# Optimization experiments

Hardware: AMD Instinct MI355X
Metric: run time of the kernel (lower is better)

Reference implementation:

```python
import jax, jax.numpy as jnp
import numpy as np

S = 2        # subsample_rate
EPS = 1e-5   # BatchNorm eps


def maxpool(x, k):
    B, C, H, W = x.shape
    return x.reshape(B, C, H // k, k, W // k, k).max(axis=(3, 5))


def conv1x1(x, w, b):
    # x: [B,C,H,W], w: [O,C], b: [O]
    return jnp.einsum('bchw,oc->bohw', x, w) + b[None, :, None, None]


def upsample_bilinear_ac(y, s):
    # torch nn.Upsample(mode='bilinear', scale_factor=s, align_corners=True)
    B, C, h, w = y.shape
    H, W = h * s, w * s
    ri = jnp.arange(H, dtype=jnp.float32) * ((h - 1) / (H - 1))
    ci = jnp.arange(W, dtype=jnp.float32) * ((w - 1) / (W - 1))
    r0 = jnp.floor(ri).astype(jnp.int32); r1 = jnp.minimum(r0 + 1, h - 1)
    c0 = jnp.floor(ci).astype(jnp.int32); c1 = jnp.minimum(c0 + 1, w - 1)
    wr = (ri - r0)[None, None, :, None]
    wc = (ci - c0)[None, None, None, :]
    top = y[:, :, r0, :] * (1.0 - wr) + y[:, :, r1, :] * wr
    return top[:, :, :, c0] * (1.0 - wc) + top[:, :, :, c1] * wc


def setup_inputs() -> dict:
    key = jax.random.key(0)
    ks = jax.random.split(key, 12)
    B, C, IC, H, W = 4, 256, 128, 192, 192
    sc = 0.05  # keep attention logits in a sane range
    x = jax.random.normal(ks[0], (B, C, H, W), jnp.float32)
    g_w = jax.random.normal(ks[1], (IC, C), jnp.float32) * sc
    g_b = jax.random.normal(ks[2], (IC,), jnp.float32) * sc
    theta_w = jax.random.normal(ks[3], (IC, C), jnp.float32) * sc
    theta_b = jax.random.normal(ks[4], (IC,), jnp.float32) * sc
    phi_w = jax.random.normal(ks[5], (IC, C), jnp.float32) * sc
    phi_b = jax.random.normal(ks[6], (IC,), jnp.float32) * sc
    W_w = jax.random.normal(ks[7], (C, IC, 3, 3), jnp.float32) * sc
    W_b = jax.random.normal(ks[8], (C,), jnp.float32) * sc
    bn_gamma = jnp.ones((C,), jnp.float32)
    bn_beta = jnp.zeros((C,), jnp.float32)
    bn_mean = jax.random.normal(ks[9], (C,), jnp.float32) * sc
    bn_var = jax.random.uniform(ks[10], (C,), jnp.float32) + 0.5
    return dict(x=x, g_w=g_w, g_b=g_b, theta_w=theta_w, theta_b=theta_b,
                phi_w=phi_w, phi_b=phi_b, W_w=W_w, W_b=W_b,
                bn_gamma=bn_gamma, bn_beta=bn_beta, bn_mean=bn_mean, bn_var=bn_var)


def reference(x, g_w, g_b, theta_w, theta_b, phi_w, phi_b, W_w, W_b,
              bn_gamma, bn_beta, bn_mean, bn_var):
    B, C, H, Wd = x.shape
    IC = g_w.shape[0]
    xp = maxpool(x, S)                               # [B,C,H/S,W/S]
    theta = conv1x1(xp, theta_w, theta_b)            # [B,IC,h,w]
    g = maxpool(conv1x1(xp, g_w, g_b), 2)            # [B,IC,h/2,w/2]
    phi = maxpool(conv1x1(xp, phi_w, phi_b), 2)      # [B,IC,h/2,w/2]
    h, w = theta.shape[2], theta.shape[3]
    th = theta.reshape(B, IC, h * w).transpose(0, 2, 1)   # [B,Nt,IC]
    ph = phi.reshape(B, IC, -1)                           # [B,IC,Np]
    gx = g.reshape(B, IC, -1).transpose(0, 2, 1)          # [B,Np,IC]
    f = jnp.einsum('bnc,bcm->bnm', th, ph)                # [B,Nt,Np]
    a = jax.nn.softmax(f, axis=-1)
    y = jnp.einsum('bnm,bmc->bnc', a, gx)                 # [B,Nt,IC]
    y = y.transpose(0, 2, 1).reshape(B, IC, h, w)
    y = upsample_bilinear_ac(y, S)                        # [B,IC,H,W]
    wy = jax.lax.conv_general_dilated(
        y, W_w, (1, 1), ((1, 1), (1, 1)),
        dimension_numbers=('NCHW', 'OIHW', 'NCHW')) + W_b[None, :, None, None]
    inv = bn_gamma / jnp.sqrt(bn_var + EPS)
    wy = (wy - bn_mean[None, :, None, None]) * inv[None, :, None, None] + bn_beta[None, :, None, None]
    return (wy + x, wy)
```

## Files before the change

kernel.cpp:

```cpp
#include <hip/hip_runtime.h>
#include <hip/hip_bf16.h>
#include <math.h>

#define B_   4
#define C_   256
#define ICH  128
#define H_   192
#define W_   192
#define hs   96
#define ws2  96
#define HW   (hs*ws2)
#define HP   48
#define WP   48
#define NP   (HP*WP)
#define EPSB 1e-5f
#define PADW 194
#define TOT  ((size_t)B_*C_*H_*W_)

#define QB 64
#define KB 64
#define NT (NP/KB)
#define SM_OFF 20.0f

using bf16x8 = __attribute__((ext_vector_type(8))) short;
using f32x4  = __attribute__((ext_vector_type(4))) float;
using f32x16 = __attribute__((ext_vector_type(16))) float;

#define OFF_XPB   ((size_t)0)
#define OFF_THB   ((size_t)4718592)
#define OFF_PHB   ((size_t)7077888)
#define OFF_GBT   ((size_t)7667712)
#define OFF_WB3   ((size_t)8257536)
#define OFF_Y96N  ((size_t)8306688)
#define OFF_ST    ((size_t)13025280)
#define OFF_WT    ((size_t)13025792)
#define OFF_YPAD  ((size_t)13173248)

static __device__ __forceinline__ float b2f(unsigned short u) {
  union { unsigned int i; float f; } c; c.i = (unsigned int)u << 16; return c.f;
}

__global__ __launch_bounds__(256) void k_pool_nhwc(const float* __restrict__ x,
                                                   __hip_bfloat16* __restrict__ xpb) {
  int idx = blockIdx.x * 256 + threadIdx.x;
  int cg = idx & 31;
  int n  = (idx >> 5) % HW;
  int b  = idx / (32 * HW);
  int pi = n / ws2, pj = n % ws2;
  const float* xb = x + (((size_t)b * C_ + cg * 8) * H_ + 2 * pi) * W_ + 2 * pj;
  union { ushort u[8]; uint4 v; } pk;
#pragma unroll
  for (int cc = 0; cc < 8; ++cc) {
    const float* s = xb + (size_t)cc * H_ * W_;
    float v = fmaxf(fmaxf(s[0], s[1]), fmaxf(s[W_], s[W_ + 1]));
    __hip_bfloat16 hv = __float2bfloat16(v);
    pk.u[cc] = *(ushort*)&hv;
  }
  *(uint4*)(xpb + ((size_t)b * HW + n) * C_ + cg * 8) = pk.v;
}

__global__ __launch_bounds__(256) void k_wprep(const float* __restrict__ tw,
                                               const float* __restrict__ gw,
                                               const float* __restrict__ pw,
                                               __hip_bfloat16* __restrict__ wb3) {
  int idx = blockIdx.x * 256 + threadIdx.x;
  int set = idx >> 15; int rem = idx & 32767;
  const float* src = set == 0 ? tw : (set == 1 ? gw : pw);
  wb3[idx] = __float2bfloat16(src[rem]);
}

__global__ __launch_bounds__(256) void k_qkv2(
    const __hip_bfloat16* __restrict__ xpb,
    const __hip_bfloat16* __restrict__ wb3,
    const float* __restrict__ tb, const float* __restrict__ gb_,
    const float* __restrict__ pb_,
    __hip_bfloat16* __restrict__ thb,
    __hip_bfloat16* __restrict__ gbt,
    __hip_bfloat16* __restrict__ phb) {
  __shared__ __align__(16) char ldsX[96 * 512];
  int t = threadIdx.x;
  int lane = t & 63, li = lane & 15, g4 = lane >> 4;
  int wid = t >> 6;
  int wave_o = wid >> 1, wave_n = wid & 1;
  int ih = blockIdx.x;
  int i  = ih >> 1, half = ih & 1;
  int b  = blockIdx.y;
  const size_t xbase = (size_t)b * HW * C_;

#pragma unroll
  for (int rr = 0; rr < 12; ++rr) {
    int e = rr * 256 + t;
    int j = e >> 5, c8 = e & 31;
    int sc8 = c8 ^ (j & 7);
    int pix = (2 * i + (j & 1)) * ws2 + half * 48 + (j >> 1);
    __builtin_amdgcn_global_load_lds(
        (const __attribute__((address_space(1))) void*)(xpb + xbase + (size_t)pix * C_ + sc8 * 8),
        (__attribute__((address_space(3))) void*)(ldsX + (rr * 256 + (t & 192)) * 16),
        16, 0, 0);
  }
  asm volatile("s_waitcnt vmcnt(0)" ::: "memory");
  __builtin_amdgcn_s_barrier();

  for (int set = 0; set < 3; ++set) {
    const __hip_bfloat16* wset = wb3 + (size_t)set * 128 * 256;
    const float* bias = set == 0 ? tb : (set == 1 ? gb_ : pb_);
    f32x4 acc[4][3];
#pragma unroll
    for (int fo = 0; fo < 4; ++fo)
#pragma unroll
      for (int fq = 0; fq < 3; ++fq) acc[fo][fq] = (f32x4){0.f, 0.f, 0.f, 0.f};

    for (int step = 0; step < 4; ++step) {
      bf16x8 af[4][2];
#pragma unroll
      for (int fo = 0; fo < 4; ++fo)
#pragma unroll
        for (int ks = 0; ks < 2; ++ks) {
          int o = wave_o * 64 + fo * 16 + li;
          af[fo][ks] = *(const bf16x8*)(wset + (size_t)o * C_ + step * 64 + ks * 32 + g4 * 8);
        }
#pragma unroll
      for (int ks = 0; ks < 2; ++ks)
#pragma unroll
        for (int fq = 0; fq < 3; ++fq) {
          int j = wave_n * 48 + fq * 16 + li;
          int sl = (step * 8 + ks * 4 + g4) ^ (j & 7);
          bf16x8 bx = *(const bf16x8*)(ldsX + j * 512 + sl * 16);
#pragma unroll
          for (int fo = 0; fo < 4; ++fo)
            acc[fo][fq] = __builtin_amdgcn_mfma_f32_16x16x32_bf16(af[fo][ks], bx, acc[fo][fq], 0, 0, 0);
        }
    }

    if (set == 0) {
#pragma unroll
      for (int fo = 0; fo < 4; ++fo) {
        int ob = wave_o * 64 + fo * 16 + g4 * 4;
#pragma unroll
        for (int fq = 0; fq < 3; ++fq) {
          int j = wave_n * 48 + fq * 16 + li;
          int pix = (2 * i + (j & 1)) * ws2 + half * 48 + (j >> 1);
          union { ushort u[4]; uint2 v; } pk;
#pragma unroll
          for (int r = 0; r < 4; ++r) {
            __hip_bfloat16 hv = __float2bfloat16(acc[fo][fq][r] + bias[ob + r]);
            pk.u[r] = *(ushort*)&hv;
          }
          *(uint2*)(thb + ((size_t)b * HW + pix) * ICH + ob) = pk.v;
        }
      }
    } else {
#pragma unroll
      for (int fo = 0; fo < 4; ++fo) {
        int ob = wave_o * 64 + fo * 16 + g4 * 4;
#pragma unroll
        for (int fq = 0; fq < 3; ++fq) {
          float pv[4];
#pragma unroll
          for (int r = 0; r < 4; ++r) {
            float p = acc[fo][fq][r];
            p = fmaxf(p, __shfl_xor(p, 1, 64));
            p = fmaxf(p, __shfl_xor(p, 2, 64));
            pv[r] = p;
          }
          if ((li & 3) == 0) {
            int pc = half * 24 + wave_n * 12 + fq * 4 + (li >> 2);
            int pp = i * WP + pc;
            if (set == 1) {
#pragma unroll
              for (int r = 0; r < 4; ++r)
                gbt[((size_t)b * ICH + ob + r) * NP + pp] = __float2bfloat16(pv[r] + bias[ob + r]);
            } else {
              union { ushort u[4]; uint2 v; } pk;
#pragma unroll
              for (int r = 0; r < 4; ++r) {
                __hip_bfloat16 hv = __float2bfloat16(pv[r] + bias[ob + r]);
                pk.u[r] = *(ushort*)&hv;
              }
              *(uint2*)(phb + ((size_t)b * NP + pp) * ICH + ob) = pk.v;
            }
          }
        }
      }
    }
  }
}

__global__ __launch_bounds__(256) void k_attn_mfma(
    const __hip_bfloat16* __restrict__ thb,
    const __hip_bfloat16* __restrict__ phb,
    const __hip_bfloat16* __restrict__ gbt,
    __hip_bfloat16* __restrict__ y96b) {
  __shared__ __align__(16) char Kl[2][KB * 256];
  __shared__ __align__(16) char Vl[2][ICH * KB * 2];
  __shared__ __align__(16) char Pl[4][16 * KB * 2];
  int t = threadIdx.x;
  int lane = t & 63, li = lane & 15, g = lane >> 4;
  int w = t >> 6;
  int flat = blockIdx.x;
  int swz = (flat & 7) * 72 + (flat >> 3);
  int b  = swz / 144;
  int q0 = (swz % 144) * QB;

  bf16x8 aq[4];
  {
    const __hip_bfloat16* qp = thb + ((size_t)b * HW + q0 + w * 16 + li) * ICH + g * 8;
#pragma unroll
    for (int ks = 0; ks < 4; ++ks) aq[ks] = *(const bf16x8*)(qp + ks * 32);
  }

  f32x4 acc_o[8];
#pragma unroll
  for (int ct = 0; ct < 8; ++ct) acc_o[ct] = (f32x4){0.f, 0.f, 0.f, 0.f};
  float l_acc[4] = {0.f, 0.f, 0.f, 0.f};

  char* Pw = (char*)Pl[w];

#define STGKV(kt_, buf_)                                                        \
  {                                                                             \
    int m0_ = (kt_) * KB;                                                       \
    _Pragma("unroll")                                                           \
    for (int rr = 0; rr < 4; ++rr) {                                            \
      int e = rr * 256 + t;                                                     \
      int mm = e >> 4, ch = (e & 15) ^ (mm & 7);                                \
      __builtin_amdgcn_global_load_lds(                                         \
          (const __attribute__((address_space(1))) void*)(phb + ((size_t)b * NP + m0_ + mm) * ICH + ch * 8), \
          (__attribute__((address_space(3))) void*)(Kl[buf_] + (rr * 256 + (t & 192)) * 16), \
          16, 0, 0);                                                            \
    }                                                                           \
    _Pragma("unroll")                                                           \
    for (int rr = 0; rr < 4; ++rr) {                                            \
      int e = rr * 256 + t;                                                     \
      int c = e >> 3, ch = (e & 7) ^ (c & 7);                                   \
      __builtin_amdgcn_global_load_lds(                                         \
          (const __attribute__((address_space(1))) void*)(gbt + ((size_t)b * ICH + c) * NP + m0_ + ch * 8), \
          (__attribute__((address_space(3))) void*)(Vl[buf_] + (rr * 256 + (t & 192)) * 16), \
          16, 0, 0);                                                            \
    }                                                                           \
  }

  STGKV(0, 0)
  for (int kt = 0; kt < NT; ++kt) {
    int buf = kt & 1;
    if (kt < NT - 1) {
      STGKV(kt + 1, buf ^ 1)
      asm volatile("s_waitcnt vmcnt(8)" ::: "memory");
    } else {
      asm volatile("s_waitcnt vmcnt(0)" ::: "memory");
    }
    __builtin_amdgcn_s_barrier();

    f32x4 s[4];
#pragma unroll
    for (int mt = 0; mt < 4; ++mt) s[mt] = (f32x4){0.f, 0.f, 0.f, 0.f};
#pragma unroll
    for (int mt = 0; mt < 4; ++mt) {
      int m = mt * 16 + li;
#pragma unroll
      for (int ks = 0; ks < 4; ++ks) {
        bf16x8 bk = *(const bf16x8*)(Kl[buf] + m * 256 + ((ks * 64 + g * 16) ^ ((li & 7) << 4)));
        s[mt] = __builtin_amdgcn_mfma_f32_16x16x32_bf16(aq[ks], bk, s[mt], 0, 0, 0);
      }
    }

#pragma unroll
    for (int mt = 0; mt < 4; ++mt) {
#pragma unroll
      for (int r = 0; r < 4; ++r) {
        float p = __expf(s[mt][r] - SM_OFF);
        s[mt][r] = p;
        l_acc[r] += p;
      }
    }

#pragma unroll
    for (int mt = 0; mt < 4; ++mt) {
      int m = mt * 16 + li;
#pragma unroll
      for (int r = 0; r < 4; ++r) {
        int ql = g * 4 + r;
        __hip_bfloat16 hv = __float2bfloat16(s[mt][r]);
        *(ushort*)(Pw + ql * 128 + ((m * 2) ^ ((ql & 7) << 4))) = *(ushort*)&hv;
      }
    }

    bf16x8 pa[2];
#pragma unroll
    for (int ks = 0; ks < 2; ++ks)
      pa[ks] = *(const bf16x8*)(Pw + li * 128 + ((ks * 64 + g * 16) ^ ((li & 7) << 4)));
#pragma unroll
    for (int ct = 0; ct < 8; ++ct) {
      int c = ct * 16 + li;
#pragma unroll
      for (int ks = 0; ks < 2; ++ks) {
        bf16x8 bv = *(const bf16x8*)(Vl[buf] + c * 128 + ((ks * 64 + g * 16) ^ ((c & 7) << 4)));
        acc_o[ct] = __builtin_amdgcn_mfma_f32_16x16x32_bf16(pa[ks], bv, acc_o[ct], 0, 0, 0);
      }
    }
    __builtin_amdgcn_s_barrier();
  }

  float inv[4];
#pragma unroll
  for (int r = 0; r < 4; ++r) {
    float l = l_acc[r];
    l += __shfl_xor(l, 1, 64);
    l += __shfl_xor(l, 2, 64);
    l += __shfl_xor(l, 4, 64);
    l += __shfl_xor(l, 8, 64);
    inv[r] = 1.f / l;
  }
  __hip_bfloat16* ob = y96b + ((size_t)b * HW + q0 + w * 16 + g * 4) * ICH + li;
#pragma unroll
  for (int r = 0; r < 4; ++r)
#pragma unroll
    for (int ct = 0; ct < 8; ++ct)
      ob[(size_t)r * ICH + ct * 16] = __float2bfloat16(acc_o[ct][r] * inv[r]);
}

__global__ __launch_bounds__(256) void k_up_pad(const __hip_bfloat16* __restrict__ y96b,
                                                __hip_bfloat16* __restrict__ ypad) {
  int idx = blockIdx.x * 256 + threadIdx.x;
  int pc  = idx % PADW;
  int r2  = idx / PADW;
  int ic8 = r2 & 15;
  int r3  = r2 >> 4;
  int pr  = r3 % PADW;
  int b   = r3 / PADW;
  __hip_bfloat16* dst = ypad + (size_t)idx * 8;
  if (pr == 0 || pr == PADW - 1 || pc == 0 || pc == PADW - 1) {
    uint2 z = {0, 0};
    *(uint2*)dst = z;
    *(uint2*)(dst + 4) = z;
    return;
  }
  int p = pr - 1, q = pc - 1;
  const float sc = 95.0f / 191.0f;
  float ri = p * sc, ci = q * sc;
  int r0 = (int)ri; int r1 = min(r0 + 1, hs - 1); float wr = ri - r0;
  int c0 = (int)ci; int c1 = min(c0 + 1, ws2 - 1); float wc = ci - c0;
  const __hip_bfloat16* base = y96b + (size_t)b * HW * ICH + ic8 * 8;
  union { ushort u[4]; uint2 v; } a, bb, cc, dd, pk;
  a.v  = *(const uint2*)(base + ((size_t)r0 * ws2 + c0) * ICH);
  bb.v = *(const uint2*)(base + ((size_t)r0 * ws2 + c1) * ICH);
  cc.v = *(const uint2*)(base + ((size_t)r1 * ws2 + c0) * ICH);
  dd.v = *(const uint2*)(base + ((size_t)r1 * ws2 + c1) * ICH);
  union { ushort u[4]; uint2 v; } a2, bb2, cc2, dd2, pk2;
  a2.v  = *(const uint2*)(base + ((size_t)r0 * ws2 + c0) * ICH + 4);
  bb2.v = *(const uint2*)(base + ((size_t)r0 * ws2 + c1) * ICH + 4);
  cc2.v = *(const uint2*)(base + ((size_t)r1 * ws2 + c0) * ICH + 4);
  dd2.v = *(const uint2*)(base + ((size_t)r1 * ws2 + c1) * ICH + 4);
#pragma unroll
  for (int j = 0; j < 4; ++j) {
    float top = b2f(a.u[j]) * (1.f - wr) + b2f(cc.u[j]) * wr;
    float bot = b2f(bb.u[j]) * (1.f - wr) + b2f(dd.u[j]) * wr;
    float v = top * (1.f - wc) + bot * wc;
    __hip_bfloat16 hv = __float2bfloat16(v);
    pk.u[j] = *(ushort*)&hv;
    float top2 = b2f(a2.u[j]) * (1.f - wr) + b2f(cc2.u[j]) * wr;
    float bot2 = b2f(bb2.u[j]) * (1.f - wr) + b2f(dd2.u[j]) * wr;
    float v2 = top2 * (1.f - wc) + bot2 * wc;
    __hip_bfloat16 hv2 = __float2bfloat16(v2);
    pk2.u[j] = *(ushort*)&hv2;
  }
  *(uint2*)dst = pk.v;
  *(uint2*)(dst + 4) = pk2.v;
}

__global__ __launch_bounds__(256) void k_wt(const float* __restrict__ Ww,
                                            __hip_bfloat16* __restrict__ Wt) {
  int idx = blockIdx.x * 256 + threadIdx.x;
  int lo  = idx & 7;
  int o   = (idx >> 3) & 255;
  int ic8 = (idx >> 11) & 15;
  int tap = idx >> 15;
  int ic  = ic8 * 8 + lo;
  Wt[idx] = __float2bfloat16(Ww[(size_t)o * (ICH * 9) + ic * 9 + tap]);
}

__global__ __launch_bounds__(256) void k_bnprep(const float* __restrict__ Wb,
                                                const float* __restrict__ bg,
                                                const float* __restrict__ bb,
                                                const float* __restrict__ bm,
                                                const float* __restrict__ bv,
                                                float* __restrict__ ST) {
  int o = threadIdx.x;
  float sc = bg[o] * rsqrtf(bv[o] + EPSB);
  ST[o] = sc;
  ST[256 + o] = (Wb[o] - bm[o]) * sc + bb[o];
}

#define ABY 12288
#define BBY 4096
#define BUF (ABY + BBY)
__global__ __launch_bounds__(256) void k_conv3_mfma(
    const __hip_bfloat16* __restrict__ ypad,
    const __hip_bfloat16* __restrict__ Wt,
    const float* __restrict__ ST,
    const float* __restrict__ x,
    float* __restrict__ out) {
  __shared__ __align__(16) char ldsM[2 * BUF];
  int t = threadIdx.x;
  int lane = t & 63;
  int l31 = lane & 31, h = lane >> 5;
  int wid = t >> 6;

  int flat = blockIdx.x;
  int swz = (flat & 7) * 384 + (flat >> 3);
  int zz  = swz / 384;
  int rem = swz % 384;
  int b  = zz >> 1;
  int o0 = (zz & 1) * 128;
  int p  = rem >> 1;
  int q0 = (rem & 1) * 96;

  f32x16 acc[3];
#pragma unroll
  for (int j = 0; j < 3; ++j)
#pragma unroll
    for (int r = 0; r < 16; ++r) acc[j][r] = 0.f;

#define STG(s_, buf_)                                                           \
  {                                                                             \
    int kh_ = (s_) >> 3, icE_ = (s_) & 7;                                       \
    char* base_ = ldsM + (buf_) * BUF;                                          \
    _Pragma("unroll")                                                           \
    for (int rr = 0; rr < 3; ++rr) {                                            \
      int e = rr * 256 + t;                                                     \
      int tap_ = e >> 8, ch_ = (e >> 7) & 1, o_ = e & 127;                      \
      size_t gsl = (((size_t)(kh_ * 3 + tap_) * 16 + icE_ * 2 + ch_) * 256 + o0 + o_) * 8; \
      __builtin_amdgcn_global_load_lds(                                         \
          (const __attribute__((address_space(1))) void*)(Wt + gsl),            \
          (__attribute__((address_space(3))) void*)(base_ + (rr * 256 + (t & 192)) * 16), \
          16, 0, 0);                                                            \
    }                                                                           \
    if (t < 196) {                                                              \
      int ch_ = (t >= 98) ? 1 : 0;                                              \
      int col_ = t - ch_ * 98;                                                  \
      size_t gsl = (((size_t)(b * PADW + p + kh_) * 16 + icE_ * 2 + ch_) * PADW + q0 + col_) * 8; \
      __builtin_amdgcn_global_load_lds(                                         \
          (const __attribute__((address_space(1))) void*)(ypad + gsl),          \
          (__attribute__((address_space(3))) void*)(base_ + ABY + (t & 192) * 16), \
          16, 0, 0);                                                            \
    }                                                                           \
  }

  STG(0, 0)
  __syncthreads();
  for (int s = 0; s < 24; ++s) {
    if (s < 23) { STG(s + 1, (s + 1) & 1) }
    const char* Ab = ldsM + (s & 1) * BUF;
    const char* Bb = Ab + ABY;
#pragma unroll
    for (int kw = 0; kw < 3; ++kw) {
      bf16x8 afr = *(const bf16x8*)(Ab + (kw * 256 + h * 128 + wid * 32 + l31) * 16);
#pragma unroll
      for (int fq = 0; fq < 3; ++fq) {
        bf16x8 bfr = *(const bf16x8*)(Bb + (h * 98 + fq * 32 + l31 + kw) * 16);
        acc[fq] = __builtin_amdgcn_mfma_f32_32x32x16_bf16(afr, bfr, acc[fq], 0, 0, 0);
      }
    }
    __syncthreads();
  }

#pragma unroll
  for (int fq = 0; fq < 3; ++fq) {
#pragma unroll
    for (int r = 0; r < 16; ++r) {
      int o = o0 + wid * 32 + (r & 3) + 8 * (r >> 2) + 4 * h;
      int q = q0 + fq * 32 + l31;
      size_t oi = (((size_t)b * C_ + o) * H_ + p) * W_ + q;
      float val = acc[fq][r] * ST[o] + ST[256 + o];
      out[TOT + oi] = val;
      out[oi] = val + x[oi];
    }
  }
}

extern "C" void kernel_launch(void* const* d_in, const int* in_sizes, int n_in,
                              void* d_out, int out_size, void* d_ws, size_t ws_size,
                              hipStream_t stream) {
  const float* x    = (const float*)d_in[0];
  const float* g_w  = (const float*)d_in[1];
  const float* g_b  = (const float*)d_in[2];
  const float* th_w = (const float*)d_in[3];
  const float* th_b = (const float*)d_in[4];
  const float* ph_w = (const float*)d_in[5];
  const float* ph_b = (const float*)d_in[6];
  const float* W_w  = (const float*)d_in[7];
  const float* W_b  = (const float*)d_in[8];
  const float* bn_g = (const float*)d_in[9];
  const float* bn_b = (const float*)d_in[10];
  const float* bn_m = (const float*)d_in[11];
  const float* bn_v = (const float*)d_in[12];
  float* out = (float*)d_out;
  float* ws  = (float*)d_ws;

  __hip_bfloat16* xpb = (__hip_bfloat16*)(ws + OFF_XPB);
  __hip_bfloat16* thb = (__hip_bfloat16*)(ws + OFF_THB);
  __hip_bfloat16* phb = (__hip_bfloat16*)(ws + OFF_PHB);
  __hip_bfloat16* gbt = (__hip_bfloat16*)(ws + OFF_GBT);
  __hip_bfloat16* wb3 = (__hip_bfloat16*)(ws + OFF_WB3);
  __hip_bfloat16* y96b = (__hip_bfloat16*)(ws + OFF_Y96N);
  float* ST   = ws + OFF_ST;
  __hip_bfloat16* Wt   = (__hip_bfloat16*)(ws + OFF_WT);
  __hip_bfloat16* ypad = (__hip_bfloat16*)(ws + OFF_YPAD);

  k_pool_nhwc<<<(B_ * HW * 32) / 256, 256, 0, stream>>>(x, xpb);
  k_wprep<<<(3 * 128 * 256) / 256, 256, 0, stream>>>(th_w, g_w, ph_w, wb3);
  k_qkv2<<<dim3(2 * HP, B_), 256, 0, stream>>>(xpb, wb3, th_b, g_b, ph_b, thb, gbt, phb);
  k_attn_mfma<<<dim3(B_ * (HW / QB)), 256, 0, stream>>>(thb, phb, gbt, y96b);
  k_up_pad<<<(B_ * PADW * 16 * PADW) / 256, 256, 0, stream>>>(y96b, ypad);
  k_wt<<<(9 * 16 * 256 * 8) / 256, 256, 0, stream>>>(W_w, Wt);
  k_bnprep<<<1, 256, 0, stream>>>(W_b, bn_g, bn_b, bn_m, bn_v, ST);
  k_conv3_mfma<<<dim3(3072), 256, 0, stream>>>(ypad, Wt, ST, x, out);
}
```

Measured before the change: 410.4 us.

## Process two 16-row query tiles per wave in attention kernel

Doubles the query block per workgroup from 64 to 128 rows, so each wave handles two 16-row query sub-tiles against each staged K/V tile. Each K and V fragment read from LDS is reused for two MFMAs, and each staged K/V tile serves twice as many queries, halving global K/V traffic per query. The cost is more registers for accumulators and Q fragments, a larger P buffer in LDS, and half as many workgroups (288), which may hurt occupancy or leave CUs underfilled.

```diff
diff --git a/kernel.cpp b/kernel.cpp
--- a/kernel.cpp
+++ b/kernel.cpp
@@ -17,7 +17,7 @@
 #define PADW 194
 #define TOT  ((size_t)B_*C_*H_*W_)
 
-#define QB 64
+#define QB 128
 #define KB 64
 #define NT (NP/KB)
 #define SM_OFF 20.0f
@@ -193,26 +193,29 @@
     __hip_bfloat16* __restrict__ y96b) {
   __shared__ __align__(16) char Kl[2][KB * 256];
   __shared__ __align__(16) char Vl[2][ICH * KB * 2];
-  __shared__ __align__(16) char Pl[4][16 * KB * 2];
+  __shared__ __align__(16) char Pl[4][32 * KB * 2];
   int t = threadIdx.x;
   int lane = t & 63, li = lane & 15, g = lane >> 4;
   int w = t >> 6;
   int flat = blockIdx.x;
-  int swz = (flat & 7) * 72 + (flat >> 3);
-  int b  = swz / 144;
-  int q0 = (swz % 144) * QB;
-
-  bf16x8 aq[4];
-  {
-    const __hip_bfloat16* qp = thb + ((size_t)b * HW + q0 + w * 16 + li) * ICH + g * 8;
-#pragma unroll
-    for (int ks = 0; ks < 4; ++ks) aq[ks] = *(const bf16x8*)(qp + ks * 32);
-  }
-
-  f32x4 acc_o[8];
-#pragma unroll
-  for (int ct = 0; ct < 8; ++ct) acc_o[ct] = (f32x4){0.f, 0.f, 0.f, 0.f};
-  float l_acc[4] = {0.f, 0.f, 0.f, 0.f};
+  int swz = (flat & 7) * 36 + (flat >> 3);
+  int b  = swz / 72;
+  int q0 = (swz % 72) * QB;
+
+  bf16x8 aq[2][4];
+#pragma unroll
+  for (int qh = 0; qh < 2; ++qh) {
+    const __hip_bfloat16* qp = thb + ((size_t)b * HW + q0 + w * 32 + qh * 16 + li) * ICH + g * 8;
+#pragma unroll
+    for (int ks = 0; ks < 4; ++ks) aq[qh][ks] = *(const bf16x8*)(qp + ks * 32);
+  }
+
+  f32x4 acc_o[2][8];
+#pragma unroll
+  for (int qh = 0; qh < 2; ++qh)
+#pragma unroll
+    for (int ct = 0; ct < 8; ++ct) acc_o[qh][ct] = (f32x4){0.f, 0.f, 0.f, 0.f};
+  float l_acc[2][4] = {{0.f, 0.f, 0.f, 0.f}, {0.f, 0.f, 0.f, 0.f}};
 
   char* Pw = (char*)Pl[w];
 
@@ -250,72 +253,82 @@
     }
     __builtin_amdgcn_s_barrier();
 
-    f32x4 s[4];
-#pragma unroll
-    for (int mt = 0; mt < 4; ++mt) s[mt] = (f32x4){0.f, 0.f, 0.f, 0.f};
-#pragma unroll
-    for (int mt = 0; mt < 4; ++mt) {
-      int m = mt * 16 + li;
-#pragma unroll
-      for (int ks = 0; ks < 4; ++ks) {
-        bf16x8 bk = *(const bf16x8*)(Kl[buf] + m * 256 + ((ks * 64 + g * 16) ^ ((li & 7) << 4)));
-        s[mt] = __builtin_amdgcn_mfma_f32_16x16x32_bf16(aq[ks], bk, s[mt], 0, 0, 0);
-      }
-    }
-
-#pragma unroll
-    for (int mt = 0; mt < 4; ++mt) {
-#pragma unroll
-      for (int r = 0; r < 4; ++r) {
-        float p = __expf(s[mt][r] - SM_OFF);
-        s[mt][r] = p;
-        l_acc[r] += p;
-      }
-    }
-
-#pragma unroll
-    for (int mt = 0; mt < 4; ++mt) {
-      int m = mt * 16 + li;
-#pragma unroll
-      for (int r = 0; r < 4; ++r) {
-        int ql = g * 4 + r;
-        __hip_bfloat16 hv = __float2bfloat16(s[mt][r]);
-        *(ushort*)(Pw + ql * 128 + ((m * 2) ^ ((ql & 7) << 4))) = *(ushort*)&hv;
-      }
-    }
-
-    bf16x8 pa[2];
-#pragma unroll
-    for (int ks = 0; ks < 2; ++ks)
-      pa[ks] = *(const bf16x8*)(Pw + li * 128 + ((ks * 64 + g * 16) ^ ((li & 7) << 4)));
+#pragma unroll
+    for (int qh = 0; qh < 2; ++qh) {
+      f32x4 s[4];
+#pragma unroll
+      for (int mt = 0; mt < 4; ++mt) s[mt] = (f32x4){0.f, 0.f, 0.f, 0.f};
+#pragma unroll
+      for (int mt = 0; mt < 4; ++mt) {
+        int m = mt * 16 + li;
+#pragma unroll
+        for (int ks = 0; ks < 4; ++ks) {
+          bf16x8 bk = *(const bf16x8*)(Kl[buf] + m * 256 + ((ks * 64 + g * 16) ^ ((li & 7) << 4)));
+          s[mt] = __builtin_amdgcn_mfma_f32_16x16x32_bf16(aq[qh][ks], bk, s[mt], 0, 0, 0);
+        }
+      }
+
+#pragma unroll
+      for (int mt = 0; mt < 4; ++mt) {
+#pragma unroll
+        for (int r = 0; r < 4; ++r) {
+          float p = __expf(s[mt][r] - SM_OFF);
+          s[mt][r] = p;
+          l_acc[qh][r] += p;
+        }
+      }
+
+#pragma unroll
+      for (int mt = 0; mt < 4; ++mt) {
+        int m = mt * 16 + li;
+#pragma unroll
+        for (int r = 0; r < 4; ++r) {
+          int ql = g * 4 + r;
+          __hip_bfloat16 hv = __float2bfloat16(s[mt][r]);
+          *(ushort*)(Pw + (qh * 16 + ql) * 128 + ((m * 2) ^ ((ql & 7) << 4))) = *(ushort*)&hv;
+        }
+      }
+    }
+
+    bf16x8 pa[2][2];
+#pragma unroll
+    for (int qh = 0; qh < 2; ++qh)
+#pragma unroll
+      for (int ks = 0; ks < 2; ++ks)
+        pa[qh][ks] = *(const bf16x8*)(Pw + (qh * 16 + li) * 128 + ((ks * 64 + g * 16) ^ ((li & 7) << 4)));
 #pragma unroll
     for (int ct = 0; ct < 8; ++ct) {
       int c = ct * 16 + li;
 #pragma unroll
       for (int ks = 0; ks < 2; ++ks) {
         bf16x8 bv = *(const bf16x8*)(Vl[buf] + c * 128 + ((ks * 64 + g * 16) ^ ((c & 7) << 4)));
-        acc_o[ct] = __builtin_amdgcn_mfma_f32_16x16x32_bf16(pa[ks], bv, acc_o[ct], 0, 0, 0);
+#pragma unroll
+        for (int qh = 0; qh < 2; ++qh)
+          acc_o[qh][ct] = __builtin_amdgcn_mfma_f32_16x16x32_bf16(pa[qh][ks], bv, acc_o[qh][ct], 0, 0, 0);
       }
     }
     __builtin_amdgcn_s_barrier();
   }
 
-  float inv[4];
-#pragma unroll
-  for (int r = 0; r < 4; ++r) {
-    float l = l_acc[r];
-    l += __shfl_xor(l, 1, 64);
-    l += __shfl_xor(l, 2, 64);
-    l += __shfl_xor(l, 4, 64);
-    l += __shfl_xor(l, 8, 64);
-    inv[r] = 1.f / l;
-  }
-  __hip_bfloat16* ob = y96b + ((size_t)b * HW + q0 + w * 16 + g * 4) * ICH + li;
-#pragma unroll
-  for (int r = 0; r < 4; ++r)
-#pragma unroll
-    for (int ct = 0; ct < 8; ++ct)
-      ob[(size_t)r * ICH + ct * 16] = __float2bfloat16(acc_o[ct][r] * inv[r]);
+#pragma unroll
+  for (int qh = 0; qh < 2; ++qh) {
+    float inv[4];
+#pragma unroll
+    for (int r = 0; r < 4; ++r) {
+      float l = l_acc[qh][r];
+      l += __shfl_xor(l, 1, 64);
+      l += __shfl_xor(l, 2, 64);
+      l += __shfl_xor(l, 4, 64);
+      l += __shfl_xor(l, 8, 64);
+      inv[r] = 1.f / l;
+    }
+    __hip_bfloat16* ob = y96b + ((size_t)b * HW + q0 + w * 32 + qh * 16 + g * 4) * ICH + li;
+#pragma unroll
+    for (int r = 0; r < 4; ++r)
+#pragma unroll
+      for (int ct = 0; ct < 8; ++ct)
+        ob[(size_t)r * ICH + ct * 16] = __float2bfloat16(acc_o[qh][ct][r] * inv[r]);
+  }
 }
 
 __global__ __launch_bounds__(256) void k_up_pad(const __hip_bfloat16* __restrict__ y96b,
```

Measured after the change: 410.9 us. Within noise of the previous version (+0.1%).
